# Kernel optimization log

Hardware: AMD Instinct MI355X
Metric: run time of the kernel (lower is better)

## Reference

```python
import jax, jax.numpy as jnp
import numpy as np

EPS = 1e-6

def _l2normalize(x, axis=1):
    # matches torch: x / sqrt(sum(x^2) + eps)
    norm = jnp.sqrt(jnp.sum(x * x, axis=axis, keepdims=True) + EPS)
    return x / norm


def setup_inputs() -> dict:
    key = jax.random.key(0)
    k1, k2, k3 = jax.random.split(key, 3)
    B, C, H, W = 8, 64, 48, 48
    x = jax.random.normal(k1, (B, C, H, W), dtype=jnp.float32)
    v = jax.random.normal(k2, (B, C, H, W), dtype=jnp.float32)
    pos = jax.random.normal(k3, (B, C, H, W), dtype=jnp.float32)
    # learned scalar parameters (init values from the torch module)
    gamma = jnp.float32(0.0)
    beta_gamma = jnp.float32(10.0)
    sum_gamma0 = jnp.float32(0.0)
    sum_gamma1 = jnp.float32(0.0)
    return {"x": x, "v": v, "pos": pos, "gamma": gamma,
            "beta_gamma": beta_gamma, "sum_gamma0": sum_gamma0,
            "sum_gamma1": sum_gamma1}


def reference(x, v, pos, gamma, beta_gamma, sum_gamma0, sum_gamma1):
    B, C, H, W = x.shape
    N = H * W
    # q and k are computed identically in the original module; compute once.
    q = _l2normalize(x + gamma * pos, axis=1)          # [B, C, H, W]
    qf = q.reshape(B, C, N)                             # [B, C, N]
    vf = v.reshape(B, v.shape[1], N)                    # [B, Cv, N]
    # scores[b, n, m] = <q[:, n], k[:, m]>; learned temperature beta_gamma
    scores = jnp.einsum('bcn,bcm->bnm', qf, qf) * beta_gamma  # [B, N, N]
    beta = jax.nn.softmax(scores, axis=-1)              # [B, N, N]
    # o = v @ beta^T  => o[b, c, n] = sum_m v[b, c, m] * beta[b, n, m]
    o = jnp.einsum('bcm,bnm->bcn', vf, beta).reshape(B, vf.shape[1], H, W)
    e0 = jnp.exp(sum_gamma0)
    e1 = jnp.exp(sum_gamma1)
    tot = e0 + e1
    out = (e0 / tot) * o + (e1 / tot) * v
    return out, beta.reshape(B, N, H, W)
```

## Files before the change

### kernel.cpp

```cpp
#include <hip/hip_runtime.h>
#include <hip/hip_bf16.h>

#define B_  8
#define C_  64
#define N_  2304
#define TS  64
#define NT_ (N_ / TS)
#define LDP 72
#define SPL 4
#define MTS (NT_ / SPL)

typedef __attribute__((ext_vector_type(8))) short  short8;
typedef __attribute__((ext_vector_type(4))) float  floatx4;

struct Hdr { int f32mode; float gamma, bg, cmax, w0, w1; };

__device__ __forceinline__ float bf2f(unsigned short u) {
  return __uint_as_float(((unsigned int)u) << 16);
}
__device__ __forceinline__ unsigned short f2bf(float f) {
  unsigned int x = __float_as_uint(f);
  x += 0x7fff + ((x >> 16) & 1);
  return (unsigned short)(x >> 16);
}

__global__ void detect_k(const void* g, const void* bgp, const void* s0,
                         const void* s1, Hdr* h) {
  if (threadIdx.x == 0 && blockIdx.x == 0) {
    int f32 = (((const unsigned short*)bgp)[0] == 0) ? 1 : 0;
    float gamma, bg, sg0, sg1;
    if (f32) {
      gamma = ((const float*)g)[0];  bg  = ((const float*)bgp)[0];
      sg0   = ((const float*)s0)[0]; sg1 = ((const float*)s1)[0];
    } else {
      gamma = bf2f(((const unsigned short*)g)[0]);
      bg    = bf2f(((const unsigned short*)bgp)[0]);
      sg0   = bf2f(((const unsigned short*)s0)[0]);
      sg1   = bf2f(((const unsigned short*)s1)[0]);
    }
    float e0 = __expf(sg0), e1 = __expf(sg1);
    h->f32mode = f32;
    h->gamma = gamma;
    h->bg = bg;
    h->cmax = fabsf(bg);
    h->w0 = e0 / (e0 + e1);
    h->w1 = e1 / (e0 + e1);
  }
}

__global__ __launch_bounds__(64)
void prep_q(const void* __restrict__ xv, const void* __restrict__ posv,
            const Hdr* __restrict__ h, unsigned short* __restrict__ qT) {
  int t = blockIdx.x * 64 + threadIdx.x;
  int b = t / N_;
  int n = t - b * N_;
  const bool f32 = h->f32mode;
  float gamma = h->gamma;
  float vals[C_];
  float s = 0.f;
  if (f32) {
    const float* xp = (const float*)xv  + (size_t)b * C_ * N_ + n;
    const float* pp = (const float*)posv + (size_t)b * C_ * N_ + n;
#pragma unroll
    for (int c = 0; c < C_; ++c) {
      float val = xp[(size_t)c * N_] + gamma * pp[(size_t)c * N_];
      vals[c] = val;  s += val * val;
    }
  } else {
    const unsigned short* xp = (const unsigned short*)xv  + (size_t)b * C_ * N_ + n;
    const unsigned short* pp = (const unsigned short*)posv + (size_t)b * C_ * N_ + n;
#pragma unroll
    for (int c = 0; c < C_; ++c) {
      float val = bf2f(xp[(size_t)c * N_]) + gamma * bf2f(pp[(size_t)c * N_]);
      vals[c] = val;  s += val * val;
    }
  }
  float inv = rsqrtf(s + 1e-6f);
  unsigned int* qrow = reinterpret_cast<unsigned int*>(qT + (size_t)t * C_);
#pragma unroll
  for (int c = 0; c < C_; c += 2) {
    qrow[c >> 1] = (unsigned int)f2bf(vals[c] * inv)
                 | ((unsigned int)f2bf(vals[c + 1] * inv) << 16);
  }
}

__global__ __launch_bounds__(256)
void pass1_rowsum(const unsigned short* __restrict__ qT,
                  const void* __restrict__ vraw,
                  const Hdr* __restrict__ h,
                  unsigned short* __restrict__ vb,
                  float* __restrict__ rowsum_part) {
  __shared__ unsigned short qm[TS * LDP];
  int bx  = blockIdx.x;
  int tid = threadIdx.x;
  {
    int t = bx * 256 + tid;
    unsigned int* vb32 = reinterpret_cast<unsigned int*>(vb);
    if (h->f32mode) {
      const float* vf = (const float*)vraw;
#pragma unroll
      for (int k = 0; k < 2; ++k) {
        int i = t + k * 294912;
        float f0 = vf[2 * i], f1 = vf[2 * i + 1];
        vb32[i] = (unsigned int)f2bf(f0) | ((unsigned int)f2bf(f1) << 16);
      }
    } else {
      const unsigned int* v32 = (const unsigned int*)vraw;
#pragma unroll
      for (int k = 0; k < 2; ++k) {
        int i = t + k * 294912;
        vb32[i] = v32[i];
      }
    }
  }
  int s  = bx & (SPL - 1);
  int nt = (bx >> 2) % NT_;
  int b  = bx / (SPL * NT_);
  int n0 = nt * TS;
  int wave = tid >> 6;
  int lane = tid & 63;
  int quad = lane >> 4;
  int l15  = lane & 15;
  float bg = h->bg, cmax = h->cmax;
  const unsigned short* abase =
      qT + ((size_t)(b * N_ + n0 + 16 * wave + l15)) * C_ + quad * 8;
  short8 a0 = *reinterpret_cast<const short8*>(abase);
  short8 a1 = *reinterpret_cast<const short8*>(abase + 32);
  float acc[4] = {0.f, 0.f, 0.f, 0.f};
  int mt0 = s * MTS;
  for (int mt = mt0; mt < mt0 + MTS; ++mt) {
    int m0 = mt * TS;
    __syncthreads();
#pragma unroll
    for (int k = 0; k < 2; ++k) {
      int chunk = tid + 256 * k;
      int row = chunk >> 3;
      int col = (chunk & 7) * 8;
      short8 vv = *reinterpret_cast<const short8*>(
          qT + ((size_t)(b * N_ + m0 + row)) * C_ + col);
      *reinterpret_cast<short8*>(&qm[row * LDP + col]) = vv;
    }
    __syncthreads();
#pragma unroll
    for (int j = 0; j < 4; ++j) {
      short8 b0 = *reinterpret_cast<const short8*>(&qm[(j * 16 + l15) * LDP + quad * 8]);
      short8 b1 = *reinterpret_cast<const short8*>(&qm[(j * 16 + l15) * LDP + 32 + quad * 8]);
      floatx4 d = {0.f, 0.f, 0.f, 0.f};
      d = __builtin_amdgcn_mfma_f32_16x16x32_bf16(a0, b0, d, 0, 0, 0);
      d = __builtin_amdgcn_mfma_f32_16x16x32_bf16(a1, b1, d, 0, 0, 0);
#pragma unroll
      for (int r = 0; r < 4; ++r)
        acc[r] += __expf(d[r] * bg - cmax);
    }
  }
#pragma unroll
  for (int r = 0; r < 4; ++r) {
    float vv = acc[r];
    vv += __shfl_xor(vv, 1);
    vv += __shfl_xor(vv, 2);
    vv += __shfl_xor(vv, 4);
    vv += __shfl_xor(vv, 8);
    acc[r] = vv;
  }
  if (l15 == 0) {
#pragma unroll
    for (int r = 0; r < 4; ++r)
      rowsum_part[((size_t)(b * N_ + n0 + 16 * wave + quad * 4 + r)) * SPL + s]
          = acc[r];
  }
}

__global__ __launch_bounds__(256)
void pass2_attn(const unsigned short* __restrict__ qT,
                const unsigned short* __restrict__ vb,
                const Hdr* __restrict__ h,
                const float* __restrict__ rowsum_part,
                float* __restrict__ opart,
                void* __restrict__ dout) {
  __shared__ unsigned short qm[TS * LDP];
  __shared__ unsigned short vt[TS * LDP];
  __shared__ unsigned short pt[TS * LDP];
  int bx = blockIdx.x;
  int s  = bx & (SPL - 1);
  int nt = (bx >> 2) % NT_;
  int b  = bx / (SPL * NT_);
  int n0 = nt * TS;
  int tid  = threadIdx.x;
  int wave = tid >> 6;
  int lane = tid & 63;
  int quad = lane >> 4;
  int l15  = lane & 15;
  const bool f32 = h->f32mode;
  float bg = h->bg, cmax = h->cmax;
  unsigned short* out16  = (unsigned short*)dout;
  unsigned short* beta16 = out16 + (size_t)B_ * C_ * N_;
  float* beta32 = (float*)dout + (size_t)B_ * C_ * N_;

  const unsigned short* abase =
      qT + ((size_t)(b * N_ + n0 + 16 * wave + l15)) * C_ + quad * 8;
  short8 a0 = *reinterpret_cast<const short8*>(abase);
  short8 a1 = *reinterpret_cast<const short8*>(abase + 32);
  float inv[4];
#pragma unroll
  for (int r = 0; r < 4; ++r) {
    floatx4 rs = *reinterpret_cast<const floatx4*>(
        rowsum_part + ((size_t)(b * N_ + n0 + 16 * wave + quad * 4 + r)) * SPL);
    inv[r] = 1.f / (rs[0] + rs[1] + rs[2] + rs[3]);
  }
  floatx4 oacc[4] = {{0.f,0.f,0.f,0.f},{0.f,0.f,0.f,0.f},
                     {0.f,0.f,0.f,0.f},{0.f,0.f,0.f,0.f}};
  int mtb = s * MTS;
  for (int mt = mtb; mt < mtb + MTS; ++mt) {
    int m0 = mt * TS;
    __syncthreads();
#pragma unroll
    for (int k = 0; k < 2; ++k) {
      int chunk = tid + 256 * k;
      int row = chunk >> 3;
      int col = (chunk & 7) * 8;
      short8 qv = *reinterpret_cast<const short8*>(
          qT + ((size_t)(b * N_ + m0 + row)) * C_ + col);
      *reinterpret_cast<short8*>(&qm[row * LDP + col]) = qv;
      short8 vv = *reinterpret_cast<const short8*>(
          vb + ((size_t)(b * C_ + row)) * N_ + m0 + col);
      *reinterpret_cast<short8*>(&vt[row * LDP + col]) = vv;
    }
    __syncthreads();
#pragma unroll
    for (int j = 0; j < 4; ++j) {
      short8 b0 = *reinterpret_cast<const short8*>(&qm[(j * 16 + l15) * LDP + quad * 8]);
      short8 b1 = *reinterpret_cast<const short8*>(&qm[(j * 16 + l15) * LDP + 32 + quad * 8]);
      floatx4 d = {0.f, 0.f, 0.f, 0.f};
      d = __builtin_amdgcn_mfma_f32_16x16x32_bf16(a0, b0, d, 0, 0, 0);
      d = __builtin_amdgcn_mfma_f32_16x16x32_bf16(a1, b1, d, 0, 0, 0);
#pragma unroll
      for (int r = 0; r < 4; ++r) {
        float p = __expf(d[r] * bg - cmax) * inv[r];
        pt[(16 * wave + quad * 4 + r) * LDP + j * 16 + l15] = f2bf(p);
        if (f32) {
          beta32[((size_t)(b * N_ + n0 + 16 * wave + quad * 4 + r)) * N_
                 + m0 + j * 16 + l15] = p;
        }
      }
    }
    __syncthreads();
    if (!f32) {
#pragma unroll
      for (int k = 0; k < 2; ++k) {
        int chunk = tid + 256 * k;
        int row = chunk >> 3;
        int col = (chunk & 7) * 8;
        short8 pv = *reinterpret_cast<const short8*>(&pt[row * LDP + col]);
        *reinterpret_cast<short8*>(
            beta16 + ((size_t)(b * N_ + n0 + row)) * N_ + m0 + col) = pv;
      }
    }
    short8 av0 = *reinterpret_cast<const short8*>(&vt[(16 * wave + l15) * LDP + quad * 8]);
    short8 av1 = *reinterpret_cast<const short8*>(&vt[(16 * wave + l15) * LDP + 32 + quad * 8]);
#pragma unroll
    for (int j = 0; j < 4; ++j) {
      short8 bp0 = *reinterpret_cast<const short8*>(&pt[(j * 16 + l15) * LDP + quad * 8]);
      short8 bp1 = *reinterpret_cast<const short8*>(&pt[(j * 16 + l15) * LDP + 32 + quad * 8]);
      oacc[j] = __builtin_amdgcn_mfma_f32_16x16x32_bf16(av0, bp0, oacc[j], 0, 0, 0);
      oacc[j] = __builtin_amdgcn_mfma_f32_16x16x32_bf16(av1, bp1, oacc[j], 0, 0, 0);
    }
  }
  float* op = opart + (size_t)s * (B_ * C_ * N_);
#pragma unroll
  for (int j = 0; j < 4; ++j) {
#pragma unroll
    for (int r = 0; r < 4; ++r) {
      int c = 16 * wave + quad * 4 + r;
      int n = n0 + 16 * j + l15;
      op[((size_t)(b * C_ + c)) * N_ + n] = oacc[j][r];
    }
  }
}

__global__ __launch_bounds__(256)
void blend_k(const float* __restrict__ opart, const void* __restrict__ vraw,
             const Hdr* __restrict__ h, void* __restrict__ dout) {
  int t = blockIdx.x * 256 + threadIdx.x;
  const int STR = (B_ * C_ * N_) / 4;
  const floatx4* p = reinterpret_cast<const floatx4*>(opart);
  floatx4 o  = p[t];
  floatx4 o1 = p[t + STR];
  floatx4 o2 = p[t + 2 * STR];
  floatx4 o3 = p[t + 3 * STR];
#pragma unroll
  for (int k = 0; k < 4; ++k) o[k] = (o[k] + o1[k]) + (o2[k] + o3[k]);
  float w0 = h->w0, w1 = h->w1;
  if (h->f32mode) {
    floatx4 vv = reinterpret_cast<const floatx4*>(vraw)[t];
    floatx4 r;
#pragma unroll
    for (int k = 0; k < 4; ++k) r[k] = w0 * o[k] + w1 * vv[k];
    reinterpret_cast<floatx4*>(dout)[t] = r;
  } else {
    unsigned long long v64 =
        reinterpret_cast<const unsigned long long*>(vraw)[t];
    unsigned long long rr = 0;
#pragma unroll
    for (int k = 0; k < 4; ++k) {
      float vf = bf2f((unsigned short)(v64 >> (16 * k)));
      rr |= ((unsigned long long)f2bf(w0 * o[k] + w1 * vf)) << (16 * k);
    }
    reinterpret_cast<unsigned long long*>(dout)[t] = rr;
  }
}

extern "C" void kernel_launch(void* const* d_in, const int* in_sizes, int n_in,
                              void* d_out, int out_size, void* d_ws, size_t ws_size,
                              hipStream_t stream) {
  const void* x     = d_in[0];
  const void* v     = d_in[1];
  const void* pos   = d_in[2];
  const void* gamma = d_in[3];
  const void* bg    = d_in[4];
  const void* sg0   = d_in[5];
  const void* sg1   = d_in[6];

  char* ws = (char*)d_ws;
  Hdr* hdr = (Hdr*)ws;
  unsigned short* qT = (unsigned short*)(ws + 256);
  unsigned short* vb = qT + (size_t)B_ * N_ * C_;
  float* rowsum_part = (float*)(ws + 256 + (size_t)B_ * N_ * C_ * 4);
  float* opart = rowsum_part + (size_t)B_ * N_ * SPL;

  detect_k<<<dim3(1), dim3(64), 0, stream>>>(gamma, bg, sg0, sg1, hdr);
  prep_q<<<dim3((B_ * N_) / 64), dim3(64), 0, stream>>>(x, pos, hdr, qT);
  pass1_rowsum<<<dim3(B_ * NT_ * SPL), dim3(256), 0, stream>>>(qT, v, hdr, vb, rowsum_part);
  pass2_attn<<<dim3(B_ * NT_ * SPL), dim3(256), 0, stream>>>(qT, vb, hdr, rowsum_part, opart, d_out);
  blend_k<<<dim3((B_ * C_ * N_) / 1024), dim3(256), 0, stream>>>(opart, v, hdr, d_out);
}
```

Before: 225.1 us.

## Inline parameter loading, split prep_q over channels, raise KV split, load V directly

Removes the single-thread header kernel and has every kernel decode the scalar parameters itself, which saves one launch. prep_q now uses 256 threads per block, with four channel groups combining their partial sums of squares through shared memory. The KV split factor rises from 4 to 6 for more blocks in the attention passes, and the row-sum partials move to a split-major layout. pass2 reads V operands straight from global memory rather than staging them in LDS. The larger split means more partial output traffic in the blend kernel.

Result: slower. 233.4 us (+3.7%).

```diff
diff --git a/kernel.cpp b/kernel.cpp
--- a/kernel.cpp
+++ b/kernel.cpp
@@ -7,13 +7,12 @@
 #define TS  64
 #define NT_ (N_ / TS)
 #define LDP 72
-#define SPL 4
+#define SPL 6
 #define MTS (NT_ / SPL)
+#define BN_ (B_ * N_)
 
 typedef __attribute__((ext_vector_type(8))) short  short8;
 typedef __attribute__((ext_vector_type(4))) float  floatx4;
-
-struct Hdr { int f32mode; float gamma, bg, cmax, w0, w1; };
 
 __device__ __forceinline__ float bf2f(unsigned short u) {
   return __uint_as_float(((unsigned int)u) << 16);
@@ -24,104 +23,113 @@
   return (unsigned short)(x >> 16);
 }
 
-__global__ void detect_k(const void* g, const void* bgp, const void* s0,
-                         const void* s1, Hdr* h) {
-  if (threadIdx.x == 0 && blockIdx.x == 0) {
-    int f32 = (((const unsigned short*)bgp)[0] == 0) ? 1 : 0;
-    float gamma, bg, sg0, sg1;
-    if (f32) {
-      gamma = ((const float*)g)[0];  bg  = ((const float*)bgp)[0];
-      sg0   = ((const float*)s0)[0]; sg1 = ((const float*)s1)[0];
-    } else {
-      gamma = bf2f(((const unsigned short*)g)[0]);
-      bg    = bf2f(((const unsigned short*)bgp)[0]);
-      sg0   = bf2f(((const unsigned short*)s0)[0]);
-      sg1   = bf2f(((const unsigned short*)s1)[0]);
-    }
-    float e0 = __expf(sg0), e1 = __expf(sg1);
-    h->f32mode = f32;
-    h->gamma = gamma;
-    h->bg = bg;
-    h->cmax = fabsf(bg);
-    h->w0 = e0 / (e0 + e1);
-    h->w1 = e1 / (e0 + e1);
-  }
-}
-
-__global__ __launch_bounds__(64)
+struct Params { int f32; float gamma, bg, cmax, w0, w1; };
+
+__device__ __forceinline__ Params load_params(const void* g, const void* bgp,
+                                              const void* s0, const void* s1) {
+  Params p;
+  p.f32 = (((const unsigned short*)bgp)[0] == 0) ? 1 : 0;
+  float sg0, sg1;
+  if (p.f32) {
+    p.gamma = ((const float*)g)[0];
+    p.bg    = ((const float*)bgp)[0];
+    sg0     = ((const float*)s0)[0];
+    sg1     = ((const float*)s1)[0];
+  } else {
+    p.gamma = bf2f(((const unsigned short*)g)[0]);
+    p.bg    = bf2f(((const unsigned short*)bgp)[0]);
+    sg0     = bf2f(((const unsigned short*)s0)[0]);
+    sg1     = bf2f(((const unsigned short*)s1)[0]);
+  }
+  float e0 = __expf(sg0), e1 = __expf(sg1);
+  p.cmax = fabsf(p.bg);
+  p.w0 = e0 / (e0 + e1);
+  p.w1 = e1 / (e0 + e1);
+  return p;
+}
+
+__global__ __launch_bounds__(256)
 void prep_q(const void* __restrict__ xv, const void* __restrict__ posv,
-            const Hdr* __restrict__ h, unsigned short* __restrict__ qT) {
-  int t = blockIdx.x * 64 + threadIdx.x;
+            const void* g, const void* bgp, const void* s0p, const void* s1p,
+            unsigned short* __restrict__ qT) {
+  __shared__ float part[4][64];
+  Params hp = load_params(g, bgp, s0p, s1p);
+  int tid = threadIdx.x;
+  int cg  = tid >> 6;
+  int nl  = tid & 63;
+  int t = blockIdx.x * 64 + nl;
   int b = t / N_;
   int n = t - b * N_;
-  const bool f32 = h->f32mode;
-  float gamma = h->gamma;
-  float vals[C_];
-  float s = 0.f;
-  if (f32) {
-    const float* xp = (const float*)xv  + (size_t)b * C_ * N_ + n;
-    const float* pp = (const float*)posv + (size_t)b * C_ * N_ + n;
-#pragma unroll
-    for (int c = 0; c < C_; ++c) {
-      float val = xp[(size_t)c * N_] + gamma * pp[(size_t)c * N_];
-      vals[c] = val;  s += val * val;
+  float gamma = hp.gamma;
+  float vals[16];
+  float ssq = 0.f;
+  size_t base = ((size_t)(b * C_ + cg * 16)) * N_ + n;
+  if (hp.f32) {
+    const float* xp = (const float*)xv;
+    const float* pp = (const float*)posv;
+#pragma unroll
+    for (int i = 0; i < 16; ++i) {
+      float val = xp[base + (size_t)i * N_] + gamma * pp[base + (size_t)i * N_];
+      vals[i] = val;  ssq += val * val;
     }
   } else {
-    const unsigned short* xp = (const unsigned short*)xv  + (size_t)b * C_ * N_ + n;
-    const unsigned short* pp = (const unsigned short*)posv + (size_t)b * C_ * N_ + n;
-#pragma unroll
-    for (int c = 0; c < C_; ++c) {
-      float val = bf2f(xp[(size_t)c * N_]) + gamma * bf2f(pp[(size_t)c * N_]);
-      vals[c] = val;  s += val * val;
-    }
-  }
+    const unsigned short* xp = (const unsigned short*)xv;
+    const unsigned short* pp = (const unsigned short*)posv;
+#pragma unroll
+    for (int i = 0; i < 16; ++i) {
+      float val = bf2f(xp[base + (size_t)i * N_])
+                + gamma * bf2f(pp[base + (size_t)i * N_]);
+      vals[i] = val;  ssq += val * val;
+    }
+  }
+  part[cg][nl] = ssq;
+  __syncthreads();
+  float s = (part[0][nl] + part[1][nl]) + (part[2][nl] + part[3][nl]);
   float inv = rsqrtf(s + 1e-6f);
-  unsigned int* qrow = reinterpret_cast<unsigned int*>(qT + (size_t)t * C_);
-#pragma unroll
-  for (int c = 0; c < C_; c += 2) {
-    qrow[c >> 1] = (unsigned int)f2bf(vals[c] * inv)
-                 | ((unsigned int)f2bf(vals[c + 1] * inv) << 16);
+  unsigned int* qrow =
+      reinterpret_cast<unsigned int*>(qT + (size_t)t * C_ + cg * 16);
+#pragma unroll
+  for (int i = 0; i < 8; ++i) {
+    qrow[i] = (unsigned int)f2bf(vals[2 * i] * inv)
+            | ((unsigned int)f2bf(vals[2 * i + 1] * inv) << 16);
   }
 }
 
 __global__ __launch_bounds__(256)
 void pass1_rowsum(const unsigned short* __restrict__ qT,
                   const void* __restrict__ vraw,
-                  const Hdr* __restrict__ h,
+                  const void* g, const void* bgp, const void* s0p, const void* s1p,
                   unsigned short* __restrict__ vb,
                   float* __restrict__ rowsum_part) {
   __shared__ unsigned short qm[TS * LDP];
+  Params hp = load_params(g, bgp, s0p, s1p);
   int bx  = blockIdx.x;
   int tid = threadIdx.x;
   {
+    const int NU32 = (B_ * C_ * N_) / 2;
+    const int TC   = (B_ * NT_ * SPL) * 256;
     int t = bx * 256 + tid;
     unsigned int* vb32 = reinterpret_cast<unsigned int*>(vb);
-    if (h->f32mode) {
+    if (hp.f32) {
       const float* vf = (const float*)vraw;
-#pragma unroll
-      for (int k = 0; k < 2; ++k) {
-        int i = t + k * 294912;
+      for (int i = t; i < NU32; i += TC) {
         float f0 = vf[2 * i], f1 = vf[2 * i + 1];
         vb32[i] = (unsigned int)f2bf(f0) | ((unsigned int)f2bf(f1) << 16);
       }
     } else {
       const unsigned int* v32 = (const unsigned int*)vraw;
-#pragma unroll
-      for (int k = 0; k < 2; ++k) {
-        int i = t + k * 294912;
-        vb32[i] = v32[i];
-      }
-    }
-  }
-  int s  = bx & (SPL - 1);
-  int nt = (bx >> 2) % NT_;
+      for (int i = t; i < NU32; i += TC) vb32[i] = v32[i];
+    }
+  }
+  int s  = bx % SPL;
+  int nt = (bx / SPL) % NT_;
   int b  = bx / (SPL * NT_);
   int n0 = nt * TS;
   int wave = tid >> 6;
   int lane = tid & 63;
   int quad = lane >> 4;
   int l15  = lane & 15;
-  float bg = h->bg, cmax = h->cmax;
+  float bg = hp.bg, cmax = hp.cmax;
   const unsigned short* abase =
       qT + ((size_t)(b * N_ + n0 + 16 * wave + l15)) * C_ + quad * 8;
   short8 a0 = *reinterpret_cast<const short8*>(abase);
@@ -165,7 +173,7 @@
   if (l15 == 0) {
 #pragma unroll
     for (int r = 0; r < 4; ++r)
-      rowsum_part[((size_t)(b * N_ + n0 + 16 * wave + quad * 4 + r)) * SPL + s]
+      rowsum_part[(size_t)s * BN_ + b * N_ + n0 + 16 * wave + quad * 4 + r]
           = acc[r];
   }
 }
@@ -173,16 +181,16 @@
 __global__ __launch_bounds__(256)
 void pass2_attn(const unsigned short* __restrict__ qT,
                 const unsigned short* __restrict__ vb,
-                const Hdr* __restrict__ h,
+                const void* g, const void* bgp, const void* s0p, const void* s1p,
                 const float* __restrict__ rowsum_part,
                 float* __restrict__ opart,
                 void* __restrict__ dout) {
   __shared__ unsigned short qm[TS * LDP];
-  __shared__ unsigned short vt[TS * LDP];
   __shared__ unsigned short pt[TS * LDP];
+  Params hp = load_params(g, bgp, s0p, s1p);
   int bx = blockIdx.x;
-  int s  = bx & (SPL - 1);
-  int nt = (bx >> 2) % NT_;
+  int s  = bx % SPL;
+  int nt = (bx / SPL) % NT_;
   int b  = bx / (SPL * NT_);
   int n0 = nt * TS;
   int tid  = threadIdx.x;
@@ -190,8 +198,8 @@
   int lane = tid & 63;
   int quad = lane >> 4;
   int l15  = lane & 15;
-  const bool f32 = h->f32mode;
-  float bg = h->bg, cmax = h->cmax;
+  const bool f32 = hp.f32;
+  float bg = hp.bg, cmax = hp.cmax;
   unsigned short* out16  = (unsigned short*)dout;
   unsigned short* beta16 = out16 + (size_t)B_ * C_ * N_;
   float* beta32 = (float*)dout + (size_t)B_ * C_ * N_;
@@ -203,15 +211,19 @@
   float inv[4];
 #pragma unroll
   for (int r = 0; r < 4; ++r) {
-    floatx4 rs = *reinterpret_cast<const floatx4*>(
-        rowsum_part + ((size_t)(b * N_ + n0 + 16 * wave + quad * 4 + r)) * SPL);
-    inv[r] = 1.f / (rs[0] + rs[1] + rs[2] + rs[3]);
+    int row = b * N_ + n0 + 16 * wave + quad * 4 + r;
+    float sum = 0.f;
+#pragma unroll
+    for (int ss = 0; ss < SPL; ++ss)
+      sum += rowsum_part[(size_t)ss * BN_ + row];
+    inv[r] = 1.f / sum;
   }
   floatx4 oacc[4] = {{0.f,0.f,0.f,0.f},{0.f,0.f,0.f,0.f},
                      {0.f,0.f,0.f,0.f},{0.f,0.f,0.f,0.f}};
   int mtb = s * MTS;
-  for (int mt = mtb; mt < mtb + MTS; ++mt) {
-    int m0 = mt * TS;
+  const unsigned short* vrow = vb + ((size_t)(b * C_ + 16 * wave + l15)) * N_;
+  for (int it = 0; it < MTS; ++it) {
+    int m0 = (mtb + it) * TS;
     __syncthreads();
 #pragma unroll
     for (int k = 0; k < 2; ++k) {
@@ -221,11 +233,10 @@
       short8 qv = *reinterpret_cast<const short8*>(
           qT + ((size_t)(b * N_ + m0 + row)) * C_ + col);
       *reinterpret_cast<short8*>(&qm[row * LDP + col]) = qv;
-      short8 vv = *reinterpret_cast<const short8*>(
-          vb + ((size_t)(b * C_ + row)) * N_ + m0 + col);
-      *reinterpret_cast<short8*>(&vt[row * LDP + col]) = vv;
-    }
-    __syncthreads();
+    }
+    __syncthreads();
+    short8 av0 = *reinterpret_cast<const short8*>(vrow + m0 + quad * 8);
+    short8 av1 = *reinterpret_cast<const short8*>(vrow + m0 + 32 + quad * 8);
 #pragma unroll
     for (int j = 0; j < 4; ++j) {
       short8 b0 = *reinterpret_cast<const short8*>(&qm[(j * 16 + l15) * LDP + quad * 8]);
@@ -255,8 +266,6 @@
             beta16 + ((size_t)(b * N_ + n0 + row)) * N_ + m0 + col) = pv;
       }
     }
-    short8 av0 = *reinterpret_cast<const short8*>(&vt[(16 * wave + l15) * LDP + quad * 8]);
-    short8 av1 = *reinterpret_cast<const short8*>(&vt[(16 * wave + l15) * LDP + 32 + quad * 8]);
 #pragma unroll
     for (int j = 0; j < 4; ++j) {
       short8 bp0 = *reinterpret_cast<const short8*>(&pt[(j * 16 + l15) * LDP + quad * 8]);
@@ -279,18 +288,21 @@
 
 __global__ __launch_bounds__(256)
 void blend_k(const float* __restrict__ opart, const void* __restrict__ vraw,
-             const Hdr* __restrict__ h, void* __restrict__ dout) {
+             const void* g, const void* bgp, const void* s0p, const void* s1p,
+             void* __restrict__ dout) {
+  Params hp = load_params(g, bgp, s0p, s1p);
   int t = blockIdx.x * 256 + threadIdx.x;
   const int STR = (B_ * C_ * N_) / 4;
   const floatx4* p = reinterpret_cast<const floatx4*>(opart);
-  floatx4 o  = p[t];
-  floatx4 o1 = p[t + STR];
-  floatx4 o2 = p[t + 2 * STR];
-  floatx4 o3 = p[t + 3 * STR];
-#pragma unroll
-  for (int k = 0; k < 4; ++k) o[k] = (o[k] + o1[k]) + (o2[k] + o3[k]);
-  float w0 = h->w0, w1 = h->w1;
-  if (h->f32mode) {
+  floatx4 o = p[t];
+#pragma unroll
+  for (int ss = 1; ss < SPL; ++ss) {
+    floatx4 q = p[t + (size_t)ss * STR];
+#pragma unroll
+    for (int k = 0; k < 4; ++k) o[k] += q[k];
+  }
+  float w0 = hp.w0, w1 = hp.w1;
+  if (hp.f32) {
     floatx4 vv = reinterpret_cast<const floatx4*>(vraw)[t];
     floatx4 r;
 #pragma unroll
@@ -321,15 +333,17 @@
   const void* sg1   = d_in[6];
 
   char* ws = (char*)d_ws;
-  Hdr* hdr = (Hdr*)ws;
   unsigned short* qT = (unsigned short*)(ws + 256);
   unsigned short* vb = qT + (size_t)B_ * N_ * C_;
   float* rowsum_part = (float*)(ws + 256 + (size_t)B_ * N_ * C_ * 4);
-  float* opart = rowsum_part + (size_t)B_ * N_ * SPL;
-
-  detect_k<<<dim3(1), dim3(64), 0, stream>>>(gamma, bg, sg0, sg1, hdr);
-  prep_q<<<dim3((B_ * N_) / 64), dim3(64), 0, stream>>>(x, pos, hdr, qT);
-  pass1_rowsum<<<dim3(B_ * NT_ * SPL), dim3(256), 0, stream>>>(qT, v, hdr, vb, rowsum_part);
-  pass2_attn<<<dim3(B_ * NT_ * SPL), dim3(256), 0, stream>>>(qT, vb, hdr, rowsum_part, opart, d_out);
-  blend_k<<<dim3((B_ * C_ * N_) / 1024), dim3(256), 0, stream>>>(opart, v, hdr, d_out);
-}
+  float* opart = rowsum_part + (size_t)SPL * BN_;
+
+  prep_q<<<dim3(BN_ / 64), dim3(256), 0, stream>>>(
+      x, pos, gamma, bg, sg0, sg1, qT);
+  pass1_rowsum<<<dim3(B_ * NT_ * SPL), dim3(256), 0, stream>>>(
+      qT, v, gamma, bg, sg0, sg1, vb, rowsum_part);
+  pass2_attn<<<dim3(B_ * NT_ * SPL), dim3(256), 0, stream>>>(
+      qT, vb, gamma, bg, sg0, sg1, rowsum_part, opart, d_out);
+  blend_k<<<dim3((B_ * C_ * N_) / 1024), dim3(256), 0, stream>>>(
+      opart, v, gamma, bg, sg0, sg1, d_out);
+}
```
